# Performance work log

Hardware: AMD Instinct MI355X
Metric: run time of the kernel (lower is better)

## Reference

```python
import jax, jax.numpy as jnp
import numpy as np

N, C, K, NUM_CLASS = 400000, 128, 128, 128


def setup_inputs() -> dict:
    key = jax.random.key(0)
    k1, k2, k3 = jax.random.split(key, 3)
    outputs = jax.random.normal(k1, (N, C), dtype=jnp.float32)
    labels = jax.random.randint(k2, (N,), 0, 2 * NUM_CLASS, dtype=jnp.int64 if jax.config.read('jax_enable_x64') else jnp.int32)
    global_logit = jax.random.normal(k3, (K, C), dtype=jnp.float32)
    return {"outputs": outputs, "labels": labels, "global_logit": global_logit, "k": NUM_CLASS}


def _pairwise_dist(x, protos):
    # Euclidean distance ||proto_j - x_i|| for all (i, j) without a [N,K,C] temp.
    x2 = jnp.sum(x * x, axis=1, keepdims=True)            # [N,1]
    p2 = jnp.sum(protos * protos, axis=1)[None, :]        # [1,K]
    d2 = x2 + p2 - 2.0 * (x @ protos.T)                   # [N,K]
    return jnp.sqrt(jnp.maximum(d2, 0.0))


def reference(outputs, labels, global_logit, k):
    # Rows with labels <= k-1 keep their label; rows with labels > k-1 get the
    # nearest-prototype index. Since the concatenated (labeled + pseudo-labeled)
    # set covers every row and CE-mean is order-invariant, we compute per-row
    # effective labels and a single mean cross-entropy.
    dists = _pairwise_dist(outputs, global_logit)          # [N,K]
    min_dist_labels = jnp.argmin(dists, axis=1)            # [N]
    is_labeled = labels <= (k - 1)
    labels_eff = jnp.where(is_labeled, labels, min_dist_labels)
    logp = jax.nn.log_softmax(outputs, axis=-1)            # [N,C]
    nll = -jnp.take_along_axis(logp, labels_eff[:, None].astype(jnp.int32), axis=1)[:, 0]
    return jnp.mean(nll)
```

## Files before the change

kernel.cpp:

```cpp
#include <hip/hip_runtime.h>


#define C_DIM 128
#define TILE_ROWS 64
#define NTHREADS 256
#define XSTRIDE 136
#define GRID_MAX 1536
#define NFRAG 32

typedef __bf16 bf16x8 __attribute__((ext_vector_type(8)));
typedef unsigned short ushort8 __attribute__((ext_vector_type(8)));
typedef float f32x4 __attribute__((ext_vector_type(4)));

union FragU { ushort8 u; bf16x8 b; };

__device__ __forceinline__ unsigned short f2bf(float f) {
    unsigned int u = __float_as_uint(f);
    u += 0x7fffu + ((u >> 16) & 1u);
    return (unsigned short)(u >> 16);
}
__device__ __forceinline__ float bf2f(unsigned short h) {
    return __uint_as_float(((unsigned int)h) << 16);
}
__device__ __forceinline__ unsigned f2ord(float s) {
    unsigned u = __float_as_uint(s);
    return (u & 0x80000000u) ? ~u : (u | 0x80000000u);
}
__device__ __forceinline__ float fmax4(float4 v) {
    return fmaxf(fmaxf(v.x, v.y), fmaxf(v.z, v.w));
}
__device__ __forceinline__ float esum4(float4 v, float m) {
    return __expf(v.x - m) + __expf(v.y - m) + __expf(v.z - m) + __expf(v.w - m);
}

extern "C" __global__ void __launch_bounds__(NTHREADS, 3)
ploss_main(const float* __restrict__ x, const int* __restrict__ labels,
           const float* __restrict__ protos, const int* __restrict__ kptr,
           float* __restrict__ partial, int n_tiles, int n_rows)
{
    __shared__ __attribute__((aligned(16))) unsigned short blds[NFRAG * 64 * 8];
    __shared__ __attribute__((aligned(16))) unsigned short x_lds[TILE_ROWS * XSTRIDE];
    __shared__ float lse_lds[TILE_ROWS];
    __shared__ float norm_lds[C_DIM];
    __shared__ float wsum[4];

    const int tid  = threadIdx.x;
    const int lane = tid & 63;
    const int wave = tid >> 6;
    const int l15  = lane & 15;
    const int quad = lane >> 4;
    const int r_l  = lane >> 2;
    const int c_l  = (lane & 3) * 32;
    const int wrow = wave * 16;
    const bool epi = (l15 == 0);
    const int kk = kptr[0];

    {
        const int j = tid >> 1;
        const float* pr = protos + j * C_DIM + (tid & 1) * 64;
        float s = 0.f;
#pragma unroll
        for (int c = 0; c < 64; c += 4) {
            float4 v = *(const float4*)(pr + c);
            s += v.x*v.x + v.y*v.y + v.z*v.z + v.w*v.w;
        }
        s += __shfl_xor(s, 1);
        if ((tid & 1) == 0) norm_lds[j] = s;
    }
#pragma unroll
    for (int f = 0; f < 8; ++f) {
        const int g = f * NTHREADS + tid;
        const int l = g & 63;
        const int frag = g >> 6;
        const int nt = frag >> 2, kt = frag & 3;
        const float* pp = protos + (nt * 16 + (l & 15)) * C_DIM + kt * 32 + (l >> 4) * 8;
        float4 v0 = *(const float4*)(pp);
        float4 v1 = *(const float4*)(pp + 4);
        FragU fr;
        fr.u[0]=f2bf(v0.x); fr.u[1]=f2bf(v0.y); fr.u[2]=f2bf(v0.z); fr.u[3]=f2bf(v0.w);
        fr.u[4]=f2bf(v1.x); fr.u[5]=f2bf(v1.y); fr.u[6]=f2bf(v1.z); fr.u[7]=f2bf(v1.w);
        *(ushort8*)&blds[g * 8] = fr.u;
    }
    __syncthreads();

    float p2h[8];
#pragma unroll
    for (int nt = 0; nt < 8; ++nt) p2h[nt] = 0.5f * norm_lds[nt * 16 + l15];

    float nll_acc = 0.f;

    int t = blockIdx.x;
    float4 a[8];
    int4 lab4 = {0, 0, 0, 0};
    {
        long long rb = (long long)t * TILE_ROWS + wrow + r_l;
        if (rb >= n_rows) rb = n_rows - 1;
        const float* xr = x + rb * C_DIM + c_l;
#pragma unroll
        for (int i = 0; i < 8; ++i) a[i] = *(const float4*)(xr + i * 4);
        if (epi) {
            long long lb = (long long)t * TILE_ROWS + wrow + quad * 4;
            if (lb > (long long)n_rows - 4) lb = n_rows - 4;
            lab4 = *(const int4*)(labels + lb);
        }
    }

    for (; t < n_tiles; t += gridDim.x) {
        const int tn = t + gridDim.x;
        const int tl = (tn < n_tiles) ? tn : t;
        float4 b[8];
        int4 labn4 = lab4;
        {
            long long rb = (long long)tl * TILE_ROWS + wrow + r_l;
            if (rb >= n_rows) rb = n_rows - 1;
            const float* xr = x + rb * C_DIM + c_l;
#pragma unroll
            for (int i = 0; i < 8; ++i) b[i] = *(const float4*)(xr + i * 4);
            if (epi) {
                long long lb = (long long)tl * TILE_ROWS + wrow + quad * 4;
                if (lb > (long long)n_rows - 4) lb = n_rows - 4;
                labn4 = *(const int4*)(labels + lb);
            }
        }

        float m = fmax4(a[0]);
#pragma unroll
        for (int i = 1; i < 8; ++i) m = fmaxf(m, fmax4(a[i]));
        float s = 0.f;
#pragma unroll
        for (int i = 0; i < 8; ++i) s += esum4(a[i], m);
#pragma unroll
        for (int mask = 1; mask <= 2; mask <<= 1) {
            float mo = __shfl_xor(m, mask);
            float so = __shfl_xor(s, mask);
            float nm = fmaxf(m, mo);
            s = s * __expf(m - nm) + so * __expf(mo - nm);
            m = nm;
        }
        if ((lane & 3) == 0) lse_lds[wrow + r_l] = m + __logf(s);

        ushort8* dst = (ushort8*)&x_lds[(wrow + r_l) * XSTRIDE + c_l];
#pragma unroll
        for (int i = 0; i < 4; ++i) {
            float4 v0 = a[2 * i], v1 = a[2 * i + 1];
            FragU wv;
            wv.u[0]=f2bf(v0.x); wv.u[1]=f2bf(v0.y); wv.u[2]=f2bf(v0.z); wv.u[3]=f2bf(v0.w);
            wv.u[4]=f2bf(v1.x); wv.u[5]=f2bf(v1.y); wv.u[6]=f2bf(v1.z); wv.u[7]=f2bf(v1.w);
            dst[i] = wv.u;
        }
        asm volatile("s_waitcnt lgkmcnt(0)" ::: "memory");
        __builtin_amdgcn_sched_barrier(0);

        FragU A[4];
#pragma unroll
        for (int kt = 0; kt < 4; ++kt)
            A[kt].u = *(const ushort8*)&x_lds[(wrow + l15) * XSTRIDE + kt * 32 + quad * 8];
        f32x4 acc[8];
        f32x4 zero = {0.f, 0.f, 0.f, 0.f};
#pragma unroll
        for (int nt = 0; nt < 8; ++nt) acc[nt] = zero;
#pragma unroll
        for (int kt = 0; kt < 4; ++kt) {
#pragma unroll
            for (int nt = 0; nt < 8; ++nt) {
                FragU B;
                B.u = *(const ushort8*)&blds[((nt * 4 + kt) * 64 + lane) * 8];
                acc[nt] = __builtin_amdgcn_mfma_f32_16x16x32_bf16(A[kt].b, B.b, acc[nt], 0, 0, 0);
            }
        }

        unsigned res[4];
#pragma unroll
        for (int rg = 0; rg < 4; ++rg) {
            unsigned u = 0xFFFFFFFFu;
#pragma unroll
            for (int nt = 0; nt < 8; ++nt) {
                unsigned c = (f2ord(p2h[nt] - acc[nt][rg]) & 0xFFFFFF80u)
                           | (unsigned)(nt * 16 + l15);
                u = (c < u) ? c : u;
            }
#pragma unroll
            for (int mask = 1; mask <= 8; mask <<= 1) {
                unsigned uo = __shfl_xor(u, mask);
                u = (uo < u) ? uo : u;
            }
            res[rg] = u;
        }

        if (epi) {
#pragma unroll
            for (int rg = 0; rg < 4; ++rg) {
                const int row16 = quad * 4 + rg;
                const long long grow = (long long)t * TILE_ROWS + wrow + row16;
                if (grow < n_rows) {
                    int lab;
                    if      (rg == 0) lab = lab4.x;
                    else if (rg == 1) lab = lab4.y;
                    else if (rg == 2) lab = lab4.z;
                    else              lab = lab4.w;
                    const int bj  = (int)(res[rg] & 127u);
                    const int eff = (lab <= kk - 1) ? lab : bj;
                    const float xv = bf2f(x_lds[(wrow + row16) * XSTRIDE + eff]);
                    nll_acc += lse_lds[wrow + row16] - xv;
                }
            }
        }

#pragma unroll
        for (int i = 0; i < 8; ++i) a[i] = b[i];
        lab4 = labn4;
    }

    float v = nll_acc;
#pragma unroll
    for (int mask = 1; mask <= 32; mask <<= 1) v += __shfl_xor(v, mask);
    if (lane == 0) wsum[wave] = v;
    __syncthreads();
    if (tid == 0) partial[blockIdx.x] = wsum[0] + wsum[1] + wsum[2] + wsum[3];
}

extern "C" __global__ void __launch_bounds__(256)
ploss_finalize(const float* __restrict__ partial, float* __restrict__ out,
               float inv_n, int nparts)
{
    __shared__ double sm[4];
    const int tid = threadIdx.x, lane = tid & 63, wave = tid >> 6;
    double v = 0.0;
    for (int i = tid; i < nparts; i += 256) v += (double)partial[i];
#pragma unroll
    for (int mask = 1; mask <= 32; mask <<= 1) v += __shfl_xor(v, mask);
    if (lane == 0) sm[wave] = v;
    __syncthreads();
    if (tid == 0) out[0] = (float)((sm[0] + sm[1] + sm[2] + sm[3]) * (double)inv_n);
}

extern "C" void kernel_launch(void* const* d_in, const int* in_sizes, int n_in,
                              void* d_out, int out_size, void* d_ws, size_t ws_size,
                              hipStream_t stream)
{
    const float* x      = (const float*)d_in[0];
    const int*   labels = (const int*)d_in[1];
    const float* protos = (const float*)d_in[2];
    const int*   kptr   = (const int*)d_in[3];
    const int n_rows  = in_sizes[0] / C_DIM;
    const int n_tiles = (n_rows + TILE_ROWS - 1) / TILE_ROWS;

    float* partial = (float*)d_ws;

    int grid = GRID_MAX;
    if (grid > n_tiles) grid = n_tiles;
    const int max_parts = (int)(ws_size / sizeof(float));
    if (grid > max_parts) grid = max_parts;
    if (grid < 1) grid = 1;

    ploss_main<<<grid, NTHREADS, 0, stream>>>(x, labels, protos, kptr, partial,
                                              n_tiles, n_rows);
    ploss_finalize<<<1, 256, 0, stream>>>(partial, (float*)d_out,
                                          1.0f / (float)n_rows, grid);
}
```

Measured before the change: 298.3 us.

## Load x directly in MFMA fragment layout, drop LDS staging of activations

Each lane now loads the x row slice that matches its MFMA A-fragment layout, so the bf16 conversion feeds the matrix instructions straight from registers. This removes the x tile and log-sum-exp round trip through LDS. The row max, sum-exp and squared norm are reduced with cross-quad shuffles. The argmin key now adds the row norm so distances stay non-negative, allowing a plain float-bits compare. The GEMM is split into two passes of four accumulators to cut register pressure, occupancy rises to 4 blocks, and the grid shrinks. The label logit is re-read from global memory in fp32 instead of from the bf16 LDS copy, which adds a scattered global load per row.

```diff
diff --git a/kernel.cpp b/kernel.cpp
--- a/kernel.cpp
+++ b/kernel.cpp
@@ -4,8 +4,7 @@
 #define C_DIM 128
 #define TILE_ROWS 64
 #define NTHREADS 256
-#define XSTRIDE 136
-#define GRID_MAX 1536
+#define GRID_MAX 1024
 #define NFRAG 32
 
 typedef __bf16 bf16x8 __attribute__((ext_vector_type(8)));
@@ -19,28 +18,28 @@
     u += 0x7fffu + ((u >> 16) & 1u);
     return (unsigned short)(u >> 16);
 }
-__device__ __forceinline__ float bf2f(unsigned short h) {
-    return __uint_as_float(((unsigned int)h) << 16);
-}
-__device__ __forceinline__ unsigned f2ord(float s) {
-    unsigned u = __float_as_uint(s);
-    return (u & 0x80000000u) ? ~u : (u | 0x80000000u);
-}
 __device__ __forceinline__ float fmax4(float4 v) {
     return fmaxf(fmaxf(v.x, v.y), fmaxf(v.z, v.w));
 }
 __device__ __forceinline__ float esum4(float4 v, float m) {
     return __expf(v.x - m) + __expf(v.y - m) + __expf(v.z - m) + __expf(v.w - m);
 }
-
-extern "C" __global__ void __launch_bounds__(NTHREADS, 3)
+__device__ __forceinline__ float dot4(float4 v) {
+    return v.x*v.x + v.y*v.y + v.z*v.z + v.w*v.w;
+}
+__device__ __forceinline__ bf16x8 cvt8(float4 lo, float4 hi) {
+    bf16x8 r;
+    r[0]=(__bf16)lo.x; r[1]=(__bf16)lo.y; r[2]=(__bf16)lo.z; r[3]=(__bf16)lo.w;
+    r[4]=(__bf16)hi.x; r[5]=(__bf16)hi.y; r[6]=(__bf16)hi.z; r[7]=(__bf16)hi.w;
+    return r;
+}
+
+extern "C" __global__ void __launch_bounds__(NTHREADS, 4)
 ploss_main(const float* __restrict__ x, const int* __restrict__ labels,
            const float* __restrict__ protos, const int* __restrict__ kptr,
            float* __restrict__ partial, int n_tiles, int n_rows)
 {
     __shared__ __attribute__((aligned(16))) unsigned short blds[NFRAG * 64 * 8];
-    __shared__ __attribute__((aligned(16))) unsigned short x_lds[TILE_ROWS * XSTRIDE];
-    __shared__ float lse_lds[TILE_ROWS];
     __shared__ float norm_lds[C_DIM];
     __shared__ float wsum[4];
 
@@ -49,11 +48,8 @@
     const int wave = tid >> 6;
     const int l15  = lane & 15;
     const int quad = lane >> 4;
-    const int r_l  = lane >> 2;
-    const int c_l  = (lane & 3) * 32;
     const int wrow = wave * 16;
-    const bool epi = (l15 == 0);
-    const int kk = kptr[0];
+    const int kk   = kptr[0];
 
     {
         const int j = tid >> 1;
@@ -62,7 +58,7 @@
 #pragma unroll
         for (int c = 0; c < 64; c += 4) {
             float4 v = *(const float4*)(pr + c);
-            s += v.x*v.x + v.y*v.y + v.z*v.z + v.w*v.w;
+            s += dot4(v);
         }
         s += __shfl_xor(s, 1);
         if ((tid & 1) == 0) norm_lds[j] = s;
@@ -91,17 +87,18 @@
 
     int t = blockIdx.x;
     float4 a[8];
-    int4 lab4 = {0, 0, 0, 0};
+    int lab = 0;
     {
-        long long rb = (long long)t * TILE_ROWS + wrow + r_l;
+        long long rb = (long long)t * TILE_ROWS + wrow + l15;
         if (rb >= n_rows) rb = n_rows - 1;
-        const float* xr = x + rb * C_DIM + c_l;
-#pragma unroll
-        for (int i = 0; i < 8; ++i) a[i] = *(const float4*)(xr + i * 4);
-        if (epi) {
-            long long lb = (long long)t * TILE_ROWS + wrow + quad * 4;
-            if (lb > (long long)n_rows - 4) lb = n_rows - 4;
-            lab4 = *(const int4*)(labels + lb);
+        const float* xr = x + rb * C_DIM;
+#pragma unroll
+        for (int i = 0; i < 8; ++i)
+            a[i] = *(const float4*)(xr + (i >> 1) * 32 + quad * 8 + (i & 1) * 4);
+        if (l15 < 4) {
+            long long lb = (long long)t * TILE_ROWS + wrow + quad * 4 + l15;
+            if (lb >= n_rows) lb = n_rows - 1;
+            lab = labels[lb];
         }
     }
 
@@ -109,106 +106,107 @@
         const int tn = t + gridDim.x;
         const int tl = (tn < n_tiles) ? tn : t;
         float4 b[8];
-        int4 labn4 = lab4;
+        int labn = lab;
         {
-            long long rb = (long long)tl * TILE_ROWS + wrow + r_l;
+            long long rb = (long long)tl * TILE_ROWS + wrow + l15;
             if (rb >= n_rows) rb = n_rows - 1;
-            const float* xr = x + rb * C_DIM + c_l;
-#pragma unroll
-            for (int i = 0; i < 8; ++i) b[i] = *(const float4*)(xr + i * 4);
-            if (epi) {
-                long long lb = (long long)tl * TILE_ROWS + wrow + quad * 4;
-                if (lb > (long long)n_rows - 4) lb = n_rows - 4;
-                labn4 = *(const int4*)(labels + lb);
+            const float* xr = x + rb * C_DIM;
+#pragma unroll
+            for (int i = 0; i < 8; ++i)
+                b[i] = *(const float4*)(xr + (i >> 1) * 32 + quad * 8 + (i & 1) * 4);
+            if (l15 < 4) {
+                long long lb = (long long)tl * TILE_ROWS + wrow + quad * 4 + l15;
+                if (lb >= n_rows) lb = n_rows - 1;
+                labn = labels[lb];
             }
         }
 
         float m = fmax4(a[0]);
 #pragma unroll
         for (int i = 1; i < 8; ++i) m = fmaxf(m, fmax4(a[i]));
-        float s = 0.f;
-#pragma unroll
-        for (int i = 0; i < 8; ++i) s += esum4(a[i], m);
-#pragma unroll
-        for (int mask = 1; mask <= 2; mask <<= 1) {
-            float mo = __shfl_xor(m, mask);
-            float so = __shfl_xor(s, mask);
-            float nm = fmaxf(m, mo);
-            s = s * __expf(m - nm) + so * __expf(mo - nm);
-            m = nm;
-        }
-        if ((lane & 3) == 0) lse_lds[wrow + r_l] = m + __logf(s);
-
-        ushort8* dst = (ushort8*)&x_lds[(wrow + r_l) * XSTRIDE + c_l];
-#pragma unroll
-        for (int i = 0; i < 4; ++i) {
-            float4 v0 = a[2 * i], v1 = a[2 * i + 1];
-            FragU wv;
-            wv.u[0]=f2bf(v0.x); wv.u[1]=f2bf(v0.y); wv.u[2]=f2bf(v0.z); wv.u[3]=f2bf(v0.w);
-            wv.u[4]=f2bf(v1.x); wv.u[5]=f2bf(v1.y); wv.u[6]=f2bf(v1.z); wv.u[7]=f2bf(v1.w);
-            dst[i] = wv.u;
-        }
-        asm volatile("s_waitcnt lgkmcnt(0)" ::: "memory");
-        __builtin_amdgcn_sched_barrier(0);
+        m = fmaxf(m, __shfl_xor(m, 16));
+        m = fmaxf(m, __shfl_xor(m, 32));
+        float s = 0.f, h2 = 0.f;
+#pragma unroll
+        for (int i = 0; i < 8; ++i) { s += esum4(a[i], m); h2 += dot4(a[i]); }
+        s  += __shfl_xor(s, 16);  h2 += __shfl_xor(h2, 16);
+        s  += __shfl_xor(s, 32);  h2 += __shfl_xor(h2, 32);
+        const float lse = m + __logf(s);
+        h2 *= 0.5f;
 
         FragU A[4];
 #pragma unroll
-        for (int kt = 0; kt < 4; ++kt)
-            A[kt].u = *(const ushort8*)&x_lds[(wrow + l15) * XSTRIDE + kt * 32 + quad * 8];
-        f32x4 acc[8];
-        f32x4 zero = {0.f, 0.f, 0.f, 0.f};
-#pragma unroll
-        for (int nt = 0; nt < 8; ++nt) acc[nt] = zero;
-#pragma unroll
-        for (int kt = 0; kt < 4; ++kt) {
-#pragma unroll
-            for (int nt = 0; nt < 8; ++nt) {
-                FragU B;
-                B.u = *(const ushort8*)&blds[((nt * 4 + kt) * 64 + lane) * 8];
-                acc[nt] = __builtin_amdgcn_mfma_f32_16x16x32_bf16(A[kt].b, B.b, acc[nt], 0, 0, 0);
-            }
-        }
-
-        unsigned res[4];
-#pragma unroll
-        for (int rg = 0; rg < 4; ++rg) {
-            unsigned u = 0xFFFFFFFFu;
-#pragma unroll
-            for (int nt = 0; nt < 8; ++nt) {
-                unsigned c = (f2ord(p2h[nt] - acc[nt][rg]) & 0xFFFFFF80u)
-                           | (unsigned)(nt * 16 + l15);
-                u = (c < u) ? c : u;
-            }
-#pragma unroll
-            for (int mask = 1; mask <= 8; mask <<= 1) {
-                unsigned uo = __shfl_xor(u, mask);
-                u = (uo < u) ? uo : u;
-            }
-            res[rg] = u;
-        }
-
-        if (epi) {
-#pragma unroll
-            for (int rg = 0; rg < 4; ++rg) {
-                const int row16 = quad * 4 + rg;
-                const long long grow = (long long)t * TILE_ROWS + wrow + row16;
-                if (grow < n_rows) {
-                    int lab;
-                    if      (rg == 0) lab = lab4.x;
-                    else if (rg == 1) lab = lab4.y;
-                    else if (rg == 2) lab = lab4.z;
-                    else              lab = lab4.w;
-                    const int bj  = (int)(res[rg] & 127u);
-                    const int eff = (lab <= kk - 1) ? lab : bj;
-                    const float xv = bf2f(x_lds[(wrow + row16) * XSTRIDE + eff]);
-                    nll_acc += lse_lds[wrow + row16] - xv;
-                }
+        for (int kt = 0; kt < 4; ++kt) A[kt].b = cvt8(a[2 * kt], a[2 * kt + 1]);
+
+        float hp[4];
+#pragma unroll
+        for (int rg = 0; rg < 4; ++rg) hp[rg] = __shfl(h2, quad * 4 + rg);
+        const float lse_r = __shfl(lse, quad * 4 + l15);
+
+        unsigned um0 = 0xFFFFFFFFu, um1 = 0xFFFFFFFFu,
+                 um2 = 0xFFFFFFFFu, um3 = 0xFFFFFFFFu;
+#pragma unroll
+        for (int pass = 0; pass < 2; ++pass) {
+            f32x4 acc[4];
+            f32x4 zero = {0.f, 0.f, 0.f, 0.f};
+#pragma unroll
+            for (int nti = 0; nti < 4; ++nti) acc[nti] = zero;
+#pragma unroll
+            for (int kt = 0; kt < 4; ++kt) {
+#pragma unroll
+                for (int nti = 0; nti < 4; ++nti) {
+                    const int nt = pass * 4 + nti;
+                    FragU B;
+                    B.u = *(const ushort8*)&blds[((nt * 4 + kt) * 64 + lane) * 8];
+                    acc[nti] = __builtin_amdgcn_mfma_f32_16x16x32_bf16(
+                                   A[kt].b, B.b, acc[nti], 0, 0, 0);
+                }
+            }
+#pragma unroll
+            for (int nti = 0; nti < 4; ++nti) {
+                const int nt = pass * 4 + nti;
+                const unsigned idx = (unsigned)(nt * 16 + l15);
+                {
+                    unsigned c = (__float_as_uint((hp[0] + p2h[nt]) - acc[nti][0]) & 0xFFFFFF80u) | idx;
+                    um0 = c < um0 ? c : um0;
+                }
+                {
+                    unsigned c = (__float_as_uint((hp[1] + p2h[nt]) - acc[nti][1]) & 0xFFFFFF80u) | idx;
+                    um1 = c < um1 ? c : um1;
+                }
+                {
+                    unsigned c = (__float_as_uint((hp[2] + p2h[nt]) - acc[nti][2]) & 0xFFFFFF80u) | idx;
+                    um2 = c < um2 ? c : um2;
+                }
+                {
+                    unsigned c = (__float_as_uint((hp[3] + p2h[nt]) - acc[nti][3]) & 0xFFFFFF80u) | idx;
+                    um3 = c < um3 ? c : um3;
+                }
+            }
+        }
+#pragma unroll
+        for (int mask = 1; mask <= 8; mask <<= 1) {
+            unsigned o0 = __shfl_xor(um0, mask); um0 = o0 < um0 ? o0 : um0;
+            unsigned o1 = __shfl_xor(um1, mask); um1 = o1 < um1 ? o1 : um1;
+            unsigned o2 = __shfl_xor(um2, mask); um2 = o2 < um2 ? o2 : um2;
+            unsigned o3 = __shfl_xor(um3, mask); um3 = o3 < um3 ? o3 : um3;
+        }
+        const int rs = l15 & 3;
+        const unsigned ur = rs == 0 ? um0 : rs == 1 ? um1 : rs == 2 ? um2 : um3;
+
+        if (l15 < 4) {
+            const long long grow = (long long)t * TILE_ROWS + wrow + quad * 4 + l15;
+            if (grow < n_rows) {
+                const int bj  = (int)(ur & 127u);
+                const int eff = (lab <= kk - 1) ? lab : bj;
+                const float xv = x[grow * C_DIM + eff];
+                nll_acc += lse_r - xv;
             }
         }
 
 #pragma unroll
         for (int i = 0; i < 8; ++i) a[i] = b[i];
-        lab4 = labn4;
+        lab = labn;
     }
 
     float v = nll_acc;
```

Result: slower. 415.4 us (+39.2%).
